# Optimization experiments

Measured on AMD Instinct MI355X. Metric: run time of the kernel, lower is better.

## Reference

```python
import jax, jax.numpy as jnp
import numpy as np

NUM_CLASSES = 80
STRIDES = (8, 16, 32)


def bce_logits(x, t):
    # numerically stable BCEWithLogits, reduction='none'
    return jnp.maximum(x, 0.) - x * t + jnp.log1p(jnp.exp(-jnp.abs(x)))


def decode_level(feat, stride):
    # feat: [B, C, H, W] -> decoded [B, HW, C], grid x/y [HW], strides [HW]
    B, C, H, W = feat.shape
    out = feat.reshape(B, C, H * W).transpose(0, 2, 1)  # [B, HW, C]
    yv, xv = jnp.meshgrid(jnp.arange(H), jnp.arange(W), indexing='ij')
    grid = jnp.stack([xv, yv], axis=-1).reshape(-1, 2).astype(feat.dtype)  # [HW, 2]
    xy = (out[..., :2] + grid[None]) * stride
    wh = jnp.exp(out[..., 2:4]) * stride
    out = jnp.concatenate([xy, wh, out[..., 4:]], axis=-1)
    return out, grid[:, 0], grid[:, 1], jnp.full((H * W,), float(stride), feat.dtype)


def pairwise_iou_cxcywh(g, p):
    # g: [G,4] gt boxes, p: [A,4] pred boxes (cx,cy,w,h) -> [G,A]
    tl = jnp.maximum(g[:, None, :2] - g[:, None, 2:] * 0.5, p[None, :, :2] - p[None, :, 2:] * 0.5)
    br = jnp.minimum(g[:, None, :2] + g[:, None, 2:] * 0.5, p[None, :, :2] + p[None, :, 2:] * 0.5)
    area_g = g[:, 2] * g[:, 3]
    area_p = p[:, 2] * p[:, 3]
    en = jnp.all(tl < br, axis=-1)
    inter = jnp.prod(br - tl, axis=-1) * en
    return inter / (area_g[:, None] + area_p[None, :] - inter + 1e-16)


def simota_assign(gt_boxes, gt_cls, bbox_p, cls_p, obj_p, xc, yc, strides):
    # per-image SimOTA label assignment (masked, jit-friendly)
    # gt_boxes [G,4], gt_cls [G] int, bbox_p [A,4], cls_p [A,C], obj_p [A,1]
    G = gt_boxes.shape[0]
    A = bbox_p.shape[0]
    gl = gt_boxes[:, 0:1] - 0.5 * gt_boxes[:, 2:3]
    gr = gt_boxes[:, 0:1] + 0.5 * gt_boxes[:, 2:3]
    gt_ = gt_boxes[:, 1:2] - 0.5 * gt_boxes[:, 3:4]
    gb = gt_boxes[:, 1:2] + 0.5 * gt_boxes[:, 3:4]
    in_box = (xc[None] > gl) & (xc[None] < gr) & (yc[None] > gt_) & (yc[None] < gb)  # [G,A]
    r = 2.5 * strides[None]
    in_ctr = ((xc[None] > gt_boxes[:, 0:1] - r) & (xc[None] < gt_boxes[:, 0:1] + r)
              & (yc[None] > gt_boxes[:, 1:2] - r) & (yc[None] < gt_boxes[:, 1:2] + r))
    geom = in_box | in_ctr
    anchor_ok = jnp.any(geom, axis=0)        # fg_mask candidate anchors [A]
    in_both = in_box & in_ctr                # [G,A]

    ious = pairwise_iou_cxcywh(gt_boxes, bbox_p)            # [G,A]
    ious = jnp.where(anchor_ok[None], ious, 0.)
    iou_cost = -jnp.log(ious + 1e-8)

    eps = 1e-8
    p = jnp.sqrt(jax.nn.sigmoid(cls_p) * jax.nn.sigmoid(obj_p))  # [A,C]
    logp = jnp.log(p + eps)
    log1mp = jnp.log(1. - p + eps)
    base = -jnp.sum(log1mp, axis=-1)                              # [A]
    sel = (logp - log1mp)[:, gt_cls]                              # [A,G]
    cls_cost = base[None, :] - sel.T                              # [G,A] = BCE(p, onehot).sum(-1)

    cost = cls_cost + 3.0 * iou_cost + 100000.0 * (~in_both) + 1e9 * (~anchor_ok[None])

    n_cand = min(10, A)
    topk_ious = jax.lax.top_k(ious, n_cand)[0]                    # [G,10]
    dyn_k = jnp.maximum(jnp.sum(topk_ious, axis=1).astype(jnp.int32), 1)  # [G]
    rank = jnp.argsort(jnp.argsort(cost, axis=1), axis=1)         # rank of each anchor per gt
    matching = (rank < dyn_k[:, None]) & anchor_ok[None]          # [G,A] bool

    am = jnp.sum(matching, axis=0)                                # anchors matched to >1 gt
    argmin_g = jnp.argmin(cost, axis=0)                           # [A]
    best = jnp.arange(G)[:, None] == argmin_g[None]               # [G,A]
    matching = jnp.where(am[None] > 1, best, matching)

    fg = jnp.any(matching, axis=0)                                # [A]
    matched_gt = jnp.argmax(matching, axis=0)                     # [A]
    pred_iou = jnp.sum(matching * ious, axis=0)                   # [A]
    cls_t = jax.nn.one_hot(gt_cls[matched_gt], NUM_CLASSES, dtype=bbox_p.dtype) * pred_iou[:, None]
    reg_t = gt_boxes[matched_gt]                                  # [A,4]
    return fg, cls_t, reg_t


def iou_elem(p, t):
    # elementwise IoU between matched pred/target boxes (cxcywh), IOUloss 'iou'
    tl = jnp.maximum(p[..., :2] - p[..., 2:] * 0.5, t[..., :2] - t[..., 2:] * 0.5)
    br = jnp.minimum(p[..., :2] + p[..., 2:] * 0.5, t[..., :2] + t[..., 2:] * 0.5)
    ap = p[..., 2] * p[..., 3]
    ag = t[..., 2] * t[..., 3]
    en = jnp.all(tl < br, axis=-1).astype(p.dtype)
    ai = jnp.prod(br - tl, axis=-1) * en
    return ai / (ap + ag - ai + 1e-16)


def yolo_loss(feat8, feat16, feat32, labels):
    outs, xs, ys, ss = [], [], [], []
    for feat, s in zip((feat8, feat16, feat32), STRIDES):
        o, x, y, st = decode_level(feat, s)
        outs.append(o); xs.append(x); ys.append(y); ss.append(st)
    outputs = jnp.concatenate(outs, axis=1)            # [B, A, 5+C]
    x_shifts = jnp.concatenate(xs)
    y_shifts = jnp.concatenate(ys)
    strides = jnp.concatenate(ss)
    xc = (x_shifts + 0.5) * strides                    # anchor centers [A]
    yc = (y_shifts + 0.5) * strides

    bbox_preds = outputs[..., :4]
    obj_preds = outputs[..., 4]
    cls_preds = outputs[..., 5:5 + NUM_CLASSES]

    labels_sg = jax.lax.stop_gradient(labels)
    gt_boxes = labels_sg[..., :4]
    gt_cls = labels_sg[..., 4].astype(jnp.int32)

    # assignment is @torch.no_grad in the original -> stop_gradient on its inputs
    fg, cls_t, reg_t = jax.vmap(simota_assign, in_axes=(0, 0, 0, 0, 0, None, None, None))(
        gt_boxes, gt_cls,
        jax.lax.stop_gradient(bbox_preds),
        jax.lax.stop_gradient(cls_preds),
        jax.lax.stop_gradient(outputs[..., 4:5]),
        xc, yc, strides)

    fg_f = fg.astype(outputs.dtype)                    # [B, A]
    iou = iou_elem(bbox_preds, reg_t)                  # [B, A]
    loss_iou = jnp.sum(fg_f * (1. - iou ** 2))
    loss_obj = jnp.sum(bce_logits(obj_preds, fg_f))
    loss_cls = jnp.sum(fg_f[..., None] * bce_logits(cls_preds, cls_t))
    num_fg = jnp.maximum(jnp.sum(fg_f), 1.)
    loss = (5.0 * loss_iou + 0.1 * loss_obj + loss_cls) / num_fg
    return loss


def setup_inputs() -> dict:
    key = jax.random.key(0)
    k1, k2, k3, k4, k5, k6, k7 = jax.random.split(key, 7)
    B, G = 32, 30
    feat8 = jax.random.normal(k1, (B, 85, 80, 80), jnp.float32)
    feat16 = jax.random.normal(k2, (B, 85, 40, 40), jnp.float32)
    feat32 = jax.random.normal(k3, (B, 85, 20, 20), jnp.float32)
    cx = jax.random.uniform(k4, (B, G, 1), jnp.float32, 60., 580.)
    cy = jax.random.uniform(k5, (B, G, 1), jnp.float32, 60., 580.)
    wh = jax.random.uniform(k6, (B, G, 2), jnp.float32, 20., 150.)
    cls = jax.random.randint(k7, (B, G, 1), 0, NUM_CLASSES).astype(jnp.float32)
    labels = jnp.concatenate([cx, cy, wh, cls], axis=-1)   # [B, G, 5] = cx,cy,w,h,cls
    return {"feat8": feat8, "feat16": feat16, "feat32": feat32, "labels": labels}


def reference(feat8, feat16, feat32, labels):
    return yolo_loss(feat8, feat16, feat32, labels)
```

## Files before the change

### kernel.cpp

```cpp
#include <hip/hip_runtime.h>
#include <cstdint>
#include <cstddef>

#define NB 32
#define NG 30
#define NA 8400
#define NC 80
#define SELB 512
#define MGRIDX 33
#define NBLK (MGRIDX * NB)

typedef unsigned long long u64;

struct Params {
  const float* f8; const float* f16; const float* f32; const float* lab;
  float*    bbox;
  float*    objlog;
  float*    po;
  float*    base_;
  unsigned* gbits;
  unsigned* mmask;
  float*    part;
  float*    out;
};

__device__ __forceinline__ float fsigm(float x) {
  return __fdividef(1.0f, 1.0f + __expf(-x));
}

__device__ __forceinline__ void anchor_geom(int a, int& x, int& y, int& W, int& hw,
                                            float& stride, int& lvl) {
  if (a < 6400)      { W = 80; hw = 6400; stride = 8.f;  lvl = 0; int i = a;        y = i / 80; x = i - y * 80; }
  else if (a < 8000) { W = 40; hw = 1600; stride = 16.f; lvl = 1; int i = a - 6400; y = i / 40; x = i - y * 40; }
  else               { W = 20; hw = 400;  stride = 32.f; lvl = 2; int i = a - 8000; y = i / 20; x = i - y * 20; }
}

__device__ __forceinline__ float pair_iou(float px, float py, float pw, float ph,
                                          float glx, float gty, float grx, float gby,
                                          float area_g) {
  float tlx = fmaxf(glx, px - pw * 0.5f);
  float tly = fmaxf(gty, py - ph * 0.5f);
  float brx = fminf(grx, px + pw * 0.5f);
  float bry = fminf(gby, py + ph * 0.5f);
  float inter = ((tlx < brx) && (tly < bry)) ? (brx - tlx) * (bry - tly) : 0.0f;
  return __fdividef(inter, area_g + pw * ph - inter + 1e-16f);
}

__device__ __forceinline__ float cost_of(float4 pb, float po, float bs, unsigned gb,
                                         int g, float glx, float gty, float grx,
                                         float gby, float area_g, float xl,
                                         float& iou_out) {
  bool ok = (gb >> 31) & 1u;
  float iou = pair_iou(pb.x, pb.y, pb.z, pb.w, glx, gty, grx, gby, area_g);
  iou = ok ? iou : 0.0f;
  float iou_cost = -__logf(iou + 1e-8f);
  float pc = fsigm(xl);
  float pr = sqrtf(pc * po);
  float cls_cost = bs - (__logf(pr + 1e-8f) - __logf(1.0f - pr + 1e-8f));
  float c = cls_cost + 3.0f * iou_cost;
  c = c + (((gb >> g) & 1u) ? 0.0f : 100000.0f);
  c = c + (ok ? 0.0f : 1000000000.0f);
  iou_out = iou;
  return c;
}

__device__ __forceinline__ u64 packkey(float c, int a) {
  unsigned b = __float_as_uint(c);
  b = (b & 0x80000000u) ? ~b : (b | 0x80000000u);
  return ((u64)b << 32) | (unsigned)a;
}

__global__ __launch_bounds__(256) void k_stage(Params p) {
  __shared__ float sgt[NG * 5];
  int b = blockIdx.y;
  int tid = threadIdx.x;
  if (tid < NG * 5) sgt[tid] = p.lab[b * NG * 5 + tid];
  __syncthreads();
  int a = blockIdx.x * 256 + tid;
  if (a >= NA) return;
  p.mmask[b * NA + a] = 0u;

  int x, y, W, hw, lvl; float stride;
  anchor_geom(a, x, y, W, hw, stride, lvl);
  const float* f = (lvl == 0) ? p.f8 : (lvl == 1) ? p.f16 : p.f32;
  int loff = (lvl == 0) ? 0 : (lvl == 1) ? 6400 : 8000;
  int fb = b * 85 * hw + (a - loff);

  float tx = f[fb];
  float ty = f[fb + hw];
  float tw = f[fb + 2 * hw];
  float th = f[fb + 3 * hw];
  float ob = f[fb + 4 * hw];

  float px = (tx + (float)x) * stride;
  float py = (ty + (float)y) * stride;
  float pw = __expf(tw) * stride;
  float ph = __expf(th) * stride;
  ((float4*)p.bbox)[b * NA + a] = make_float4(px, py, pw, ph);
  p.objlog[b * NA + a] = ob;

  float po = fsigm(ob);
  p.po[b * NA + a] = po;
  float bs = 0.0f;
  int cb = fb + 5 * hw;
#pragma unroll 8
  for (int c = 0; c < NC; c++) {
    float xl = f[cb + c * hw];
    float pc = fsigm(xl);
    float pr = sqrtf(pc * po);
    bs -= __logf(1.0f - pr + 1e-8f);
  }
  p.base_[b * NA + a] = bs;

  float xc = ((float)x + 0.5f) * stride;
  float yc = ((float)y + 0.5f) * stride;
  float r = 2.5f * stride;
  unsigned gb = 0; int ok = 0;
#pragma unroll
  for (int g = 0; g < NG; g++) {
    float gx = sgt[g * 5], gy = sgt[g * 5 + 1], gw = sgt[g * 5 + 2], gh = sgt[g * 5 + 3];
    bool inb = (xc > gx - 0.5f * gw) && (xc < gx + 0.5f * gw) &&
               (yc > gy - 0.5f * gh) && (yc < gy + 0.5f * gh);
    bool inc = (xc > gx - r) && (xc < gx + r) && (yc > gy - r) && (yc < gy + r);
    ok |= (inb || inc) ? 1 : 0;
    gb |= (unsigned)(inb && inc) << g;
  }
  gb |= (unsigned)ok << 31;
  p.gbits[b * NA + a] = gb;
}

__device__ __forceinline__ void block_argmax(float& v, int& i, int tid,
                                             float* swv, int* swi) {
#pragma unroll
  for (int off = 32; off; off >>= 1) {
    float v2 = __shfl_down(v, off, 64);
    int   i2 = __shfl_down(i, off, 64);
    if (v2 > v) { v = v2; i = i2; }
  }
  int wv = tid >> 6;
  if ((tid & 63) == 0) { swv[wv] = v; swi[wv] = i; }
  __syncthreads();
  float bv = swv[0]; int bi = swi[0];
#pragma unroll
  for (int w = 1; w < SELB / 64; w++) {
    if (swv[w] > bv) { bv = swv[w]; bi = swi[w]; }
  }
  v = bv; i = bi;
  __syncthreads();
}

__device__ __forceinline__ u64 block_min_u64(u64 k, int tid, u64* swk) {
#pragma unroll
  for (int off = 32; off; off >>= 1) {
    u64 k2 = __shfl_down(k, off, 64);
    if (k2 < k) k = k2;
  }
  int wv = tid >> 6;
  if ((tid & 63) == 0) swk[wv] = k;
  __syncthreads();
  u64 m = swk[0];
#pragma unroll
  for (int w = 1; w < SELB / 64; w++) if (swk[w] < m) m = swk[w];
  __syncthreads();
  return m;
}

#define SCAN_ONE(A, XL)                                                   \
  {                                                                       \
    unsigned gb = gbv[(A)];                                               \
    if (gb >> 31) {                                                       \
      float4 pb = bb[(A)];                                                \
      float iou;                                                          \
      float c = cost_of(pb, pov[(A)], bsv[(A)], gb, g,                    \
                        glx, gty, grx, gby, area_g, (XL), iou);           \
      if (iou > v[9]) {                                                   \
        float nv = iou;                                                   \
        _Pragma("unroll")                                                 \
        for (int j = 0; j < 10; j++) {                                    \
          float hi = fmaxf(v[j], nv);                                     \
          nv = fminf(v[j], nv);                                           \
          v[j] = hi;                                                      \
        }                                                                 \
      }                                                                   \
      u64 nk = packkey(c, (A));                                           \
      if (nk < kv[9]) {                                                   \
        _Pragma("unroll")                                                 \
        for (int j = 0; j < 10; j++) {                                    \
          u64 lo = (kv[j] < nk) ? kv[j] : nk;                             \
          u64 hi = (kv[j] < nk) ? nk : kv[j];                             \
          kv[j] = lo; nk = hi;                                            \
        }                                                                 \
      }                                                                   \
    }                                                                     \
  }

__global__ __launch_bounds__(SELB) void k_sel(Params p) {
  __shared__ float swv[SELB / 64];
  __shared__ int   swi[SELB / 64];
  __shared__ u64   swk[SELB / 64];
  int bg = blockIdx.x;
  int b = bg / NG, g = bg % NG;
  int tid = threadIdx.x;

  const float* gt = p.lab + (b * NG + g) * 5;
  float gx = gt[0], gy = gt[1], gw = gt[2], gh = gt[3];
  int cg = (int)gt[4];
  float glx = gx - 0.5f * gw, grx = gx + 0.5f * gw;
  float gty = gy - 0.5f * gh, gby = gy + 0.5f * gh;
  float area_g = gw * gh;

  const float4*   bb = (const float4*)p.bbox + b * NA;
  const float*    pov = p.po + b * NA;
  const float*    bsv = p.base_ + b * NA;
  const unsigned* gbv = p.gbits + b * NA;

  float v[10];
  u64   kv[10];
#pragma unroll
  for (int j = 0; j < 10; j++) { v[j] = 0.0f; kv[j] = ~0ull; }

  {
    const float* f = p.f8;
    int cbase = b * 85 * 6400 + (5 + cg) * 6400;
    for (int al = tid; al < 6400; al += SELB) SCAN_ONE(al, f[cbase + al]);
  }
  {
    const float* f = p.f16;
    int cbase = b * 85 * 1600 + (5 + cg) * 1600;
    for (int al = tid; al < 1600; al += SELB) SCAN_ONE(6400 + al, f[cbase + al]);
  }
  {
    const float* f = p.f32;
    int cbase = b * 85 * 400 + (5 + cg) * 400;
    for (int al = tid; al < 400; al += SELB) SCAN_ONE(8000 + al, f[cbase + al]);
  }

  float sum = 0.0f; int ptr = 0;
  for (int it = 0; it < 10; it++) {
    float mv = (ptr < 10) ? v[ptr] : -1e30f;
    int   mi = tid;
    block_argmax(mv, mi, tid, swv, swi);
    if (tid == mi) ptr++;
    sum += mv;
  }
  int dynk = (int)sum;
  if (dynk < 1) dynk = 1;

  ptr = 0;
  unsigned* mrow = p.mmask + b * NA;
  unsigned gbit = 1u << g;
  for (int it = 0; it < dynk; it++) {
    u64 mk = (ptr < 10) ? kv[ptr] : ~0ull;
    u64 win = block_min_u64(mk, tid, swk);
    if (ptr < 10 && kv[ptr] == win) {
      if (win != ~0ull) atomicOr(&mrow[(unsigned)(win & 0xFFFFFFFFu)], gbit);
      ptr++;
    }
  }
}

__device__ __forceinline__ float block_sum(float val, volatile float* sw) {
#pragma unroll
  for (int off = 32; off > 0; off >>= 1) val += __shfl_down(val, off, 64);
  int lane = threadIdx.x & 63, wv = threadIdx.x >> 6;
  __syncthreads();
  if (lane == 0) sw[wv] = val;
  __syncthreads();
  float r = 0.0f;
  if (threadIdx.x == 0) r = sw[0] + sw[1] + sw[2] + sw[3];
  return r;
}

__global__ __launch_bounds__(256) void k_match(Params p) {
  __shared__ float sred[4];
  int b = blockIdx.y;
  int tid = threadIdx.x;
  int lane = tid & 63;
  int a = blockIdx.x * 256 + tid;
  bool valid = a < NA;

  float l_iou = 0.0f, l_obj = 0.0f, l_cls = 0.0f, l_nfg = 0.0f;
  unsigned mask = 0; int am = 0;
  bool fg = false; float pred_iou = 0.0f; int cg_ = 0;

  if (valid) {
    mask = p.mmask[b * NA + a];
    am = __popc(mask);
    fg = (mask != 0u);
    float ol = p.objlog[b * NA + a];
    float tfg = fg ? 1.0f : 0.0f;
    l_obj = fmaxf(ol, 0.0f) - ol * tfg + __logf(1.0f + __expf(-fabsf(ol)));
  }

  unsigned long long amb = __ballot(valid && am > 1);
  while (amb) {
    int src = __ffsll(amb) - 1;
    amb &= amb - 1ull;
    int aa = __shfl(a, src, 64);
    float4 pb = ((const float4*)p.bbox)[b * NA + aa];
    float po_ = p.po[b * NA + aa];
    float bs_ = p.base_[b * NA + aa];
    unsigned gb_ = p.gbits[b * NA + aa];

    int lvl = (aa < 6400) ? 0 : (aa < 8000) ? 1 : 2;
    int hw  = (lvl == 0) ? 6400 : (lvl == 1) ? 1600 : 400;
    int loff = (lvl == 0) ? 0 : (lvl == 1) ? 6400 : 8000;
    const float* f = (lvl == 0) ? p.f8 : (lvl == 1) ? p.f16 : p.f32;
    int cb = b * 85 * hw + 5 * hw + (aa - loff);

    float c = 3.4e38f; int gg = 0x7FFFFFFF;
    if (lane < NG) {
      const float* gtg = p.lab + (b * NG + lane) * 5;
      float gx = gtg[0], gy = gtg[1], gw = gtg[2], gh = gtg[3];
      int cg = (int)gtg[4];
      float xl = f[cb + cg * hw];
      float iou_;
      c = cost_of(pb, po_, bs_, gb_, lane,
                  gx - 0.5f * gw, gy - 0.5f * gh,
                  gx + 0.5f * gw, gy + 0.5f * gh, gw * gh, xl, iou_);
      gg = lane;
    }
#pragma unroll
    for (int off = 32; off; off >>= 1) {
      float c2 = __shfl_down(c, off, 64);
      int   g2 = __shfl_down(gg, off, 64);
      if (c2 < c || (c2 == c && g2 < gg)) { c = c2; gg = g2; }
    }
    gg = __shfl(gg, 0, 64);
    if (lane == src) mask = 1u << gg;
  }

  if (valid && fg) {
    l_nfg = 1.0f;
    int mg = __ffs(mask) - 1;
    const float* gtm = p.lab + (b * NG + mg) * 5;
    float gx = gtm[0], gy = gtm[1], gw = gtm[2], gh = gtm[3];
    cg_ = (int)gtm[4];
    float4 pb = ((const float4*)p.bbox)[b * NA + a];
    float iou = pair_iou(pb.x, pb.y, pb.z, pb.w,
                         gx - 0.5f * gw, gy - 0.5f * gh,
                         gx + 0.5f * gw, gy + 0.5f * gh, gw * gh);
    pred_iou = iou;
    l_iou = 1.0f - iou * iou;
  }

  unsigned long long fgb = __ballot(valid && fg);
  while (fgb) {
    int src = __ffsll(fgb) - 1;
    fgb &= fgb - 1ull;
    int   aa   = __shfl(a, src, 64);
    float piou = __shfl(pred_iou, src, 64);
    int   ccg  = __shfl(cg_, src, 64);

    int lvl = (aa < 6400) ? 0 : (aa < 8000) ? 1 : 2;
    int hw  = (lvl == 0) ? 6400 : (lvl == 1) ? 1600 : 400;
    int loff = (lvl == 0) ? 0 : (lvl == 1) ? 6400 : 8000;
    const float* f = (lvl == 0) ? p.f8 : (lvl == 1) ? p.f16 : p.f32;
    int cb = b * 85 * hw + 5 * hw + (aa - loff);

    float part = 0.0f;
#pragma unroll
    for (int c0 = 0; c0 < NC; c0 += 64) {
      int c = c0 + lane;
      if (c < NC) {
        float xl = f[cb + c * hw];
        float t = (c == ccg) ? piou : 0.0f;
        part += fmaxf(xl, 0.0f) - xl * t + __logf(1.0f + __expf(-fabsf(xl)));
      }
    }
#pragma unroll
    for (int off = 32; off; off >>= 1) part += __shfl_down(part, off, 64);
    if (lane == 0) l_cls += part;
  }

  float s0 = block_sum(l_iou, sred);
  float s1 = block_sum(l_obj, sred);
  float s2 = block_sum(l_cls, sred);
  float s3 = block_sum(l_nfg, sred);
  if (tid == 0) {
    ((float4*)p.part)[b * MGRIDX + blockIdx.x] = make_float4(s0, s1, s2, s3);
  }
}

__global__ __launch_bounds__(256) void k_final(Params p) {
  __shared__ float sred[4];
  int tid = threadIdx.x;
  float s0 = 0.0f, s1 = 0.0f, s2 = 0.0f, s3 = 0.0f;
  for (int i = tid; i < NBLK; i += 256) {
    float4 v = ((const float4*)p.part)[i];
    s0 += v.x; s1 += v.y; s2 += v.z; s3 += v.w;
  }
  s0 = block_sum(s0, sred);
  s1 = block_sum(s1, sred);
  s2 = block_sum(s2, sred);
  s3 = block_sum(s3, sred);
  if (tid == 0) {
    p.out[0] = (5.0f * s0 + 0.1f * s1 + s2) / fmaxf(s3, 1.0f);
  }
}

extern "C" void kernel_launch(void* const* d_in, const int* in_sizes, int n_in,
                              void* d_out, int out_size, void* d_ws, size_t ws_size,
                              hipStream_t stream) {
  Params p;
  p.f8  = (const float*)d_in[0];
  p.f16 = (const float*)d_in[1];
  p.f32 = (const float*)d_in[2];
  p.lab = (const float*)d_in[3];

  float* w = (float*)d_ws;
  p.bbox   = w;              w += (size_t)NB * NA * 4;
  p.objlog = w;              w += (size_t)NB * NA;
  p.po     = w;              w += (size_t)NB * NA;
  p.base_  = w;              w += (size_t)NB * NA;
  p.gbits  = (unsigned*)w;   w += (size_t)NB * NA;
  p.mmask  = (unsigned*)w;   w += (size_t)NB * NA;
  p.part   = w;              w += (size_t)NBLK * 4;
  p.out    = (float*)d_out;

  dim3 gd(MGRIDX, NB);
  k_stage<<<gd, 256, 0, stream>>>(p);
  k_sel<<<NB * NG, SELB, 0, stream>>>(p);
  k_match<<<gd, 256, 0, stream>>>(p);
  k_final<<<1, 256, 0, stream>>>(p);
}
```

Before: 217.7 us.

## Compact candidate anchors and compute class base cost only for in-both anchors

The 80-class base cost is no longer computed for every anchor. k_stage now builds per-image lists of anchors that lie both in a GT box and in its centre region, and k_base computes the base cost only for those. k_sel compacts the IoU values of box-overlapping anchors into shared memory for the top-10 dynamic-k sum, and ranks costs only over the per-GT in-both candidate list. A slow fallback scan handles the case where that list holds fewer than dynamic-k anchors, and the new atomics and fixed list capacities add complexity and the risk of overflow.

```diff
diff --git a/kernel.cpp b/kernel.cpp
--- a/kernel.cpp
+++ b/kernel.cpp
@@ -9,6 +9,9 @@
 #define SELB 512
 #define MGRIDX 33
 #define NBLK (MGRIDX * NB)
+#define CAP 80
+#define DCAP 2304
+#define NITER 17
 
 typedef unsigned long long u64;
 
@@ -19,7 +22,12 @@
   float*    po;
   float*    base_;
   unsigned* gbits;
+  unsigned* obits;
   unsigned* mmask;
+  unsigned* cand;
+  unsigned* ccount;
+  unsigned* dcount;
+  unsigned* dlist;
   float*    part;
   float*    out;
 };
@@ -70,6 +78,28 @@
   return ((u64)b << 32) | (unsigned)a;
 }
 
+__device__ float base_of(const Params& p, int b, int a, float po) {
+  int lvl = (a < 6400) ? 0 : (a < 8000) ? 1 : 2;
+  int hw  = (lvl == 0) ? 6400 : (lvl == 1) ? 1600 : 400;
+  int loff = (lvl == 0) ? 0 : (lvl == 1) ? 6400 : 8000;
+  const float* f = (lvl == 0) ? p.f8 : (lvl == 1) ? p.f16 : p.f32;
+  int cb = b * 85 * hw + 5 * hw + (a - loff);
+  float bs = 0.0f;
+#pragma unroll 1
+  for (int c = 0; c < NC; c++) {
+    float xl = f[cb + c * hw];
+    float pc = fsigm(xl);
+    float pr = sqrtf(pc * po);
+    bs -= __logf(1.0f - pr + 1e-8f);
+  }
+  return bs;
+}
+
+__global__ __launch_bounds__(256) void k_zero(Params p) {
+  int i = blockIdx.x * 256 + threadIdx.x;
+  if (i < NB * NG + NB) p.ccount[i] = 0u;
+}
+
 __global__ __launch_bounds__(256) void k_stage(Params p) {
   __shared__ float sgt[NG * 5];
   int b = blockIdx.y;
@@ -98,11 +128,53 @@
   float ph = __expf(th) * stride;
   ((float4*)p.bbox)[b * NA + a] = make_float4(px, py, pw, ph);
   p.objlog[b * NA + a] = ob;
-
-  float po = fsigm(ob);
-  p.po[b * NA + a] = po;
+  p.po[b * NA + a] = fsigm(ob);
+
+  float xc = ((float)x + 0.5f) * stride;
+  float yc = ((float)y + 0.5f) * stride;
+  float r = 2.5f * stride;
+  float plx = px - 0.5f * pw, prx = px + 0.5f * pw;
+  float pty = py - 0.5f * ph, pby = py + 0.5f * ph;
+  unsigned gb = 0, ov = 0; int ok = 0;
+#pragma unroll
+  for (int g = 0; g < NG; g++) {
+    float gx = sgt[g * 5], gy = sgt[g * 5 + 1], gw = sgt[g * 5 + 2], gh = sgt[g * 5 + 3];
+    float glx = gx - 0.5f * gw, grx = gx + 0.5f * gw;
+    float gty_ = gy - 0.5f * gh, gby = gy + 0.5f * gh;
+    bool inb = (xc > glx) && (xc < grx) && (yc > gty_) && (yc < gby);
+    bool inc = (xc > gx - r) && (xc < gx + r) && (yc > gy - r) && (yc < gy + r);
+    ok |= (inb || inc) ? 1 : 0;
+    bool ib = inb && inc;
+    gb |= (unsigned)ib << g;
+    bool o = (fmaxf(glx, plx) < fminf(grx, prx)) && (fmaxf(gty_, pty) < fminf(gby, pby));
+    ov |= (unsigned)o << g;
+    if (ib) {
+      unsigned slot = atomicAdd(&p.ccount[b * NG + g], 1u);
+      if (slot < CAP) p.cand[(b * NG + g) * CAP + slot] = (unsigned)a;
+    }
+  }
+  gb |= (unsigned)ok << 31;
+  p.gbits[b * NA + a] = gb;
+  p.obits[b * NA + a] = ok ? ov : 0u;
+  if (gb & 0x3FFFFFFFu) {
+    unsigned s = atomicAdd(&p.dcount[b], 1u);
+    if (s < DCAP) p.dlist[b * DCAP + s] = (unsigned)a;
+  }
+}
+
+__global__ __launch_bounds__(256) void k_base(Params p) {
+  int b = blockIdx.y;
+  unsigned n = p.dcount[b]; if (n > DCAP) n = DCAP;
+  unsigned i = blockIdx.x * 256 + threadIdx.x;
+  if (i >= n) return;
+  int a = (int)p.dlist[b * DCAP + i];
+  int lvl = (a < 6400) ? 0 : (a < 8000) ? 1 : 2;
+  int hw  = (lvl == 0) ? 6400 : (lvl == 1) ? 1600 : 400;
+  int loff = (lvl == 0) ? 0 : (lvl == 1) ? 6400 : 8000;
+  const float* f = (lvl == 0) ? p.f8 : (lvl == 1) ? p.f16 : p.f32;
+  int cb = b * 85 * hw + 5 * hw + (a - loff);
+  float po = p.po[b * NA + a];
   float bs = 0.0f;
-  int cb = fb + 5 * hw;
 #pragma unroll 8
   for (int c = 0; c < NC; c++) {
     float xl = f[cb + c * hw];
@@ -111,42 +183,6 @@
     bs -= __logf(1.0f - pr + 1e-8f);
   }
   p.base_[b * NA + a] = bs;
-
-  float xc = ((float)x + 0.5f) * stride;
-  float yc = ((float)y + 0.5f) * stride;
-  float r = 2.5f * stride;
-  unsigned gb = 0; int ok = 0;
-#pragma unroll
-  for (int g = 0; g < NG; g++) {
-    float gx = sgt[g * 5], gy = sgt[g * 5 + 1], gw = sgt[g * 5 + 2], gh = sgt[g * 5 + 3];
-    bool inb = (xc > gx - 0.5f * gw) && (xc < gx + 0.5f * gw) &&
-               (yc > gy - 0.5f * gh) && (yc < gy + 0.5f * gh);
-    bool inc = (xc > gx - r) && (xc < gx + r) && (yc > gy - r) && (yc < gy + r);
-    ok |= (inb || inc) ? 1 : 0;
-    gb |= (unsigned)(inb && inc) << g;
-  }
-  gb |= (unsigned)ok << 31;
-  p.gbits[b * NA + a] = gb;
-}
-
-__device__ __forceinline__ void block_argmax(float& v, int& i, int tid,
-                                             float* swv, int* swi) {
-#pragma unroll
-  for (int off = 32; off; off >>= 1) {
-    float v2 = __shfl_down(v, off, 64);
-    int   i2 = __shfl_down(i, off, 64);
-    if (v2 > v) { v = v2; i = i2; }
-  }
-  int wv = tid >> 6;
-  if ((tid & 63) == 0) { swv[wv] = v; swi[wv] = i; }
-  __syncthreads();
-  float bv = swv[0]; int bi = swi[0];
-#pragma unroll
-  for (int w = 1; w < SELB / 64; w++) {
-    if (swv[w] > bv) { bv = swv[w]; bi = swi[w]; }
-  }
-  v = bv; i = bi;
-  __syncthreads();
 }
 
 __device__ __forceinline__ u64 block_min_u64(u64 k, int tid, u64* swk) {
@@ -165,42 +201,17 @@
   return m;
 }
 
-#define SCAN_ONE(A, XL)                                                   \
-  {                                                                       \
-    unsigned gb = gbv[(A)];                                               \
-    if (gb >> 31) {                                                       \
-      float4 pb = bb[(A)];                                                \
-      float iou;                                                          \
-      float c = cost_of(pb, pov[(A)], bsv[(A)], gb, g,                    \
-                        glx, gty, grx, gby, area_g, (XL), iou);           \
-      if (iou > v[9]) {                                                   \
-        float nv = iou;                                                   \
-        _Pragma("unroll")                                                 \
-        for (int j = 0; j < 10; j++) {                                    \
-          float hi = fmaxf(v[j], nv);                                     \
-          nv = fminf(v[j], nv);                                           \
-          v[j] = hi;                                                      \
-        }                                                                 \
-      }                                                                   \
-      u64 nk = packkey(c, (A));                                           \
-      if (nk < kv[9]) {                                                   \
-        _Pragma("unroll")                                                 \
-        for (int j = 0; j < 10; j++) {                                    \
-          u64 lo = (kv[j] < nk) ? kv[j] : nk;                             \
-          u64 hi = (kv[j] < nk) ? nk : kv[j];                             \
-          kv[j] = lo; nk = hi;                                            \
-        }                                                                 \
-      }                                                                   \
-    }                                                                     \
-  }
-
 __global__ __launch_bounds__(SELB) void k_sel(Params p) {
+  __shared__ float sh_iou[NA];
   __shared__ float swv[SELB / 64];
   __shared__ int   swi[SELB / 64];
   __shared__ u64   swk[SELB / 64];
+  __shared__ int   sh_excl[10];
+  __shared__ int   scnt;
   int bg = blockIdx.x;
   int b = bg / NG, g = bg % NG;
   int tid = threadIdx.x;
+  if (tid == 0) scnt = 0;
 
   const float* gt = p.lab + (b * NG + g) * 5;
   float gx = gt[0], gy = gt[1], gw = gt[2], gh = gt[3];
@@ -208,53 +219,128 @@
   float glx = gx - 0.5f * gw, grx = gx + 0.5f * gw;
   float gty = gy - 0.5f * gh, gby = gy + 0.5f * gh;
   float area_g = gw * gh;
-
-  const float4*   bb = (const float4*)p.bbox + b * NA;
-  const float*    pov = p.po + b * NA;
-  const float*    bsv = p.base_ + b * NA;
-  const unsigned* gbv = p.gbits + b * NA;
-
-  float v[10];
-  u64   kv[10];
-#pragma unroll
-  for (int j = 0; j < 10; j++) { v[j] = 0.0f; kv[j] = ~0ull; }
-
-  {
-    const float* f = p.f8;
-    int cbase = b * 85 * 6400 + (5 + cg) * 6400;
-    for (int al = tid; al < 6400; al += SELB) SCAN_ONE(al, f[cbase + al]);
-  }
-  {
-    const float* f = p.f16;
-    int cbase = b * 85 * 1600 + (5 + cg) * 1600;
-    for (int al = tid; al < 1600; al += SELB) SCAN_ONE(6400 + al, f[cbase + al]);
-  }
-  {
-    const float* f = p.f32;
-    int cbase = b * 85 * 400 + (5 + cg) * 400;
-    for (int al = tid; al < 400; al += SELB) SCAN_ONE(8000 + al, f[cbase + al]);
-  }
-
-  float sum = 0.0f; int ptr = 0;
-  for (int it = 0; it < 10; it++) {
-    float mv = (ptr < 10) ? v[ptr] : -1e30f;
-    int   mi = tid;
-    block_argmax(mv, mi, tid, swv, swi);
-    if (tid == mi) ptr++;
-    sum += mv;
+  const float4*   bb  = (const float4*)p.bbox + b * NA;
+  const unsigned* obv = p.obits + b * NA;
+  __syncthreads();
+
+  unsigned obw[NITER];
+#pragma unroll
+  for (int it = 0; it < NITER; it++) {
+    int a = it * SELB + tid;
+    obw[it] = (a < NA) ? obv[a] : 0u;
+  }
+#pragma unroll
+  for (int it = 0; it < NITER; it++) {
+    int a = it * SELB + tid;
+    bool act = (obw[it] >> g) & 1u;
+    u64 bal = __ballot(act);
+    if (bal) {
+      int lane = tid & 63;
+      int leader = __ffsll(bal) - 1;
+      int basec = 0;
+      if (lane == leader) basec = atomicAdd(&scnt, __popcll(bal));
+      basec = __shfl(basec, leader, 64);
+      if (act) {
+        int pre = __popcll(bal & ((1ull << lane) - 1ull));
+        float4 pb = bb[a];
+        float iou = pair_iou(pb.x, pb.y, pb.z, pb.w, glx, gty, grx, gby, area_g);
+        sh_iou[basec + pre] = iou;
+      }
+    }
+  }
+  __syncthreads();
+  int n = scnt;
+
+  float sum = 0.0f;
+  for (int rnd = 0; rnd < 10; rnd++) {
+    float mv = -1.0f; int mi = -1;
+    for (int j = tid; j < n; j += SELB) {
+      float v = sh_iou[j];
+      if (v > mv) { mv = v; mi = j; }
+    }
+#pragma unroll
+    for (int off = 32; off; off >>= 1) {
+      float v2 = __shfl_down(mv, off, 64);
+      int   i2 = __shfl_down(mi, off, 64);
+      if (v2 > mv) { mv = v2; mi = i2; }
+    }
+    if ((tid & 63) == 0) { swv[tid >> 6] = mv; swi[tid >> 6] = mi; }
+    __syncthreads();
+    float bv = swv[0]; int bi = swi[0];
+#pragma unroll
+    for (int w = 1; w < SELB / 64; w++)
+      if (swv[w] > bv) { bv = swv[w]; bi = swi[w]; }
+    sum += fmaxf(bv, 0.0f);
+    if (tid == 0 && bi >= 0) sh_iou[bi] = -1.0f;
+    __syncthreads();
   }
   int dynk = (int)sum;
   if (dynk < 1) dynk = 1;
 
-  ptr = 0;
+  unsigned nc = p.ccount[b * NG + g]; if (nc > CAP) nc = CAP;
+  u64 key = ~0ull;
+  if (tid < (int)nc) {
+    int a = (int)p.cand[(b * NG + g) * CAP + tid];
+    float4 pb = bb[a];
+    float po_ = p.po[b * NA + a];
+    float bs_ = p.base_[b * NA + a];
+    unsigned gb_ = p.gbits[b * NA + a];
+    int lvl = (a < 6400) ? 0 : (a < 8000) ? 1 : 2;
+    int hw  = (lvl == 0) ? 6400 : (lvl == 1) ? 1600 : 400;
+    int loff = (lvl == 0) ? 0 : (lvl == 1) ? 6400 : 8000;
+    const float* f = (lvl == 0) ? p.f8 : (lvl == 1) ? p.f16 : p.f32;
+    float xl = f[b * 85 * hw + (5 + cg) * hw + (a - loff)];
+    float iou_;
+    float c = cost_of(pb, po_, bs_, gb_, g, glx, gty, grx, gby, area_g, xl, iou_);
+    key = packkey(c, a);
+  }
   unsigned* mrow = p.mmask + b * NA;
   unsigned gbit = 1u << g;
+  int matched = 0;
   for (int it = 0; it < dynk; it++) {
-    u64 mk = (ptr < 10) ? kv[ptr] : ~0ull;
-    u64 win = block_min_u64(mk, tid, swk);
-    if (ptr < 10 && kv[ptr] == win) {
-      if (win != ~0ull) atomicOr(&mrow[(unsigned)(win & 0xFFFFFFFFu)], gbit);
-      ptr++;
+    u64 win = block_min_u64(key, tid, swk);
+    if (win == ~0ull) break;
+    if (key == win) {
+      atomicOr(&mrow[(unsigned)(win & 0xFFFFFFFFu)], gbit);
+      key = ~0ull;
+    }
+    matched++;
+  }
+
+  if (matched < dynk) {
+    const unsigned* gbv = p.gbits + b * NA;
+    const float*    pov = p.po + b * NA;
+    for (int it = matched; it < dynk; it++) {
+      u64 best = ~0ull;
+      for (int al = tid; al < NA; al += SELB) {
+        unsigned gb = gbv[al];
+        if (!(gb >> 31)) continue;
+        if ((gb >> g) & 1u) continue;
+        bool skip = false;
+        for (int e = matched; e < it; e++) if (sh_excl[e] == al) skip = true;
+        if (skip) continue;
+        float po_ = pov[al];
+        float bs = base_of(p, b, al, po_);
+        int lvl = (al < 6400) ? 0 : (al < 8000) ? 1 : 2;
+        int hw  = (lvl == 0) ? 6400 : (lvl == 1) ? 1600 : 400;
+        int loff = (lvl == 0) ? 0 : (lvl == 1) ? 6400 : 8000;
+        const float* f = (lvl == 0) ? p.f8 : (lvl == 1) ? p.f16 : p.f32;
+        float xl = f[b * 85 * hw + (5 + cg) * hw + (al - loff)];
+        float4 pb = bb[al];
+        float iou_;
+        float c = cost_of(pb, po_, bs, gb, g, glx, gty, grx, gby, area_g, xl, iou_);
+        u64 nk = packkey(c, al);
+        if (nk < best) best = nk;
+      }
+      u64 win = block_min_u64(best, tid, swk);
+      if (win == ~0ull) break;
+      int aw = (int)(win & 0xFFFFFFFFu);
+      if (best == win) {
+        atomicOr(&mrow[aw], gbit);
+        p.base_[b * NA + aw] = base_of(p, b, aw, pov[aw]);
+      }
+      if (tid == 0) sh_excl[it] = aw;
+      __syncthreads();
     }
   }
 }
@@ -414,13 +500,20 @@
   p.po     = w;              w += (size_t)NB * NA;
   p.base_  = w;              w += (size_t)NB * NA;
   p.gbits  = (unsigned*)w;   w += (size_t)NB * NA;
+  p.obits  = (unsigned*)w;   w += (size_t)NB * NA;
   p.mmask  = (unsigned*)w;   w += (size_t)NB * NA;
+  p.cand   = (unsigned*)w;   w += (size_t)NB * NG * CAP;
+  p.ccount = (unsigned*)w;   w += (size_t)NB * NG;
+  p.dcount = (unsigned*)w;   w += (size_t)NB;
+  p.dlist  = (unsigned*)w;   w += (size_t)NB * DCAP;
   p.part   = w;              w += (size_t)NBLK * 4;
   p.out    = (float*)d_out;
 
   dim3 gd(MGRIDX, NB);
+  k_zero <<<dim3(4), 256, 0, stream>>>(p);
   k_stage<<<gd, 256, 0, stream>>>(p);
-  k_sel<<<NB * NG, SELB, 0, stream>>>(p);
+  k_base <<<dim3(DCAP / 256, NB), 256, 0, stream>>>(p);
+  k_sel  <<<NB * NG, SELB, 0, stream>>>(p);
   k_match<<<gd, 256, 0, stream>>>(p);
   k_final<<<1, 256, 0, stream>>>(p);
 }
```

Result: faster. 207.6 us (-4.6%).
